# Kernel tuning notes

Hardware: AMD Instinct MI355X
Metric: run time of the kernel (lower is better)

## Reference

```python
import jax, jax.numpy as jnp
import numpy as np

NUM_HEADS = 16

def setup_inputs() -> dict:
    key = jax.random.key(0)
    k1, k2, k3 = jax.random.split(key, 3)
    B, S, H = 2, 2048, 1024
    x = jax.random.normal(k1, (B, S, H), dtype=jnp.float32)
    w_qkv = jax.random.normal(k2, (H, 3 * H), dtype=jnp.float32) * (1.0 / np.sqrt(H))
    w_out = jax.random.normal(k3, (H, H), dtype=jnp.float32) * (1.0 / np.sqrt(H))
    return {"x": x, "w_qkv": w_qkv, "w_out": w_out}

def reference(x, w_qkv, w_out):
    B, S, H = x.shape
    nh = NUM_HEADS
    dh = H // nh
    qkv = x @ w_qkv  # (B, S, 3H)
    q, k, v = jnp.split(qkv, 3, axis=-1)
    # (B, nh, S, dh)
    q = q.reshape(B, S, nh, dh).transpose(0, 2, 1, 3)
    k = k.reshape(B, S, nh, dh).transpose(0, 2, 1, 3)
    v = v.reshape(B, S, nh, dh).transpose(0, 2, 1, 3)
    att = jnp.einsum('bhsd,bhSd->bhsS', q, k) / np.sqrt(dh).astype(np.float32)
    causal = jnp.tril(jnp.ones((S, S), dtype=bool))
    att = jnp.where(causal[None, None], att, -jnp.inf)
    att = jax.nn.softmax(att, axis=-1)
    out = jnp.einsum('bhsS,bhSd->bhsd', att, v)
    out = out.transpose(0, 2, 1, 3).reshape(B, S, H)
    return out @ w_out
```

## Files before the change

### kernel.cpp

```cpp
#include <hip/hip_runtime.h>

#define DEVINL __device__ __forceinline__

typedef __attribute__((ext_vector_type(8)))  __bf16         bf16x8;
typedef __attribute__((ext_vector_type(4)))  float          f32x4;
typedef __attribute__((ext_vector_type(16))) float          f32x16;
typedef __attribute__((ext_vector_type(8)))  unsigned short ushort8;
typedef __attribute__((ext_vector_type(4)))  unsigned short ushort4v;
typedef __attribute__((ext_vector_type(4)))  unsigned int   uint4v;
typedef __attribute__((ext_vector_type(4)))  float          float4v;

DEVINL unsigned short f2bf(float f) {
  unsigned int u = __float_as_uint(f);
  u += 0x7fffu + ((u >> 16) & 1u);
  return (unsigned short)(u >> 16);
}

DEVINL float bf2f(unsigned short u) {
  return __uint_as_float(((unsigned int)u) << 16);
}

DEVINL bf16x8 ldbf8(const unsigned short* p) {
  return __builtin_bit_cast(bf16x8, *(const ushort8*)p);
}

DEVINL unsigned cvtpk_bf16(float lo, float hi) {
  unsigned r;
  asm("v_cvt_pk_bf16_f32 %0, %1, %2" : "=v"(r) : "v"(lo), "v"(hi));
  return r;
}

DEVINL void gload_lds16(const unsigned short* g, unsigned short* l) {
  __builtin_amdgcn_global_load_lds((const __attribute__((address_space(1))) void*)g,
                                   (__attribute__((address_space(3))) void*)l, 16, 0, 0);
}

__global__ __launch_bounds__(256) void prepass_kernel(
    const float* __restrict__ x, const float* __restrict__ w_qkv,
    const float* __restrict__ w_out, unsigned short* __restrict__ xb,
    unsigned short* __restrict__ wqkvT, unsigned short* __restrict__ woutT) {
  __shared__ float tile[32][33];
  const int B = blockIdx.x;
  if (B < 1024) {
    const int n4 = 1048576;
    for (int i = B * 256 + threadIdx.x; i < n4; i += 1024 * 256) {
      float4v v = *(const float4v*)(x + (size_t)4 * i);
      ushort4v o;
      o[0] = f2bf(v[0]); o[1] = f2bf(v[1]); o[2] = f2bf(v[2]); o[3] = f2bf(v[3]);
      *(ushort4v*)(xb + (size_t)4 * i) = o;
    }
    return;
  }
  const float* in; unsigned short* out; int C, bx, by;
  if (B < 4096) { const int idx = B - 1024; bx = idx % 96; by = idx / 96; in = w_qkv; out = wqkvT; C = 3072; }
  else          { const int idx = B - 4096; bx = idx & 31; by = idx >> 5; in = w_out; out = woutT; C = 1024; }
  const int R = 1024;
  const int tx = threadIdx.x & 31, ty = threadIdx.x >> 5;
  const int r0 = by << 5, c0 = bx << 5;
#pragma unroll
  for (int i = 0; i < 32; i += 8)
    tile[ty + i][tx] = in[(size_t)(r0 + ty + i) * C + (c0 + tx)];
  __syncthreads();
#pragma unroll
  for (int i = 0; i < 32; i += 8)
    out[(size_t)(c0 + ty + i) * R + (r0 + tx)] = f2bf(tile[tx][ty + i]);
}

template <bool OUT_BF16>
__global__ __launch_bounds__(256, 3) void gemm_bt_kernel(
    const unsigned short* __restrict__ A,
    const unsigned short* __restrict__ Bt,
    void* __restrict__ Cout,
    int M, int N, int K, int lda, int ldb, int ldc,
    unsigned short* __restrict__ VtOut) {
  __shared__ __align__(16) unsigned short smem[2][2][128 * 32];
  unsigned short (*As)[128 * 32] = smem[0];
  unsigned short (*Bs)[128 * 32] = smem[1];
  const int tid = threadIdx.x;
  const int lane = tid & 63, wave = tid >> 6;
  const int wr = wave >> 1, wc = wave & 1;
  const int g = lane >> 4, q = lane & 15;
  const int row0 = blockIdx.x << 7, col0 = blockIdx.y << 7;

  const int srow = tid >> 2;
  const int sg = ((tid & 3) ^ (srow & 3) ^ ((srow >> 2) & 3)) << 3;
  const unsigned short* Ap0 = A + (size_t)(row0 + srow) * lda + sg;
  const unsigned short* Ap1 = Ap0 + (size_t)64 * lda;
  const unsigned short* Bp0 = Bt + (size_t)(col0 + srow) * ldb + sg;
  const unsigned short* Bp1 = Bp0 + (size_t)64 * ldb;

  f32x4 acc[4][4] = {};

  gload_lds16(Ap0, &As[0][wave * 512]);
  gload_lds16(Ap1, &As[0][2048 + wave * 512]);
  gload_lds16(Bp0, &Bs[0][wave * 512]);
  gload_lds16(Bp1, &Bs[0][2048 + wave * 512]);

  const int gx = (g ^ (q & 3) ^ (q >> 2)) << 3;
  const int nk = K >> 5;
  int cur = 0;

  for (int t = 0; t < nk; ++t) {
    if (t + 1 < nk) {
      Ap0 += 32; Ap1 += 32; Bp0 += 32; Bp1 += 32;
      gload_lds16(Ap0, &As[cur ^ 1][wave * 512]);
      gload_lds16(Ap1, &As[cur ^ 1][2048 + wave * 512]);
      gload_lds16(Bp0, &Bs[cur ^ 1][wave * 512]);
      gload_lds16(Bp1, &Bs[cur ^ 1][2048 + wave * 512]);
      asm volatile("s_waitcnt vmcnt(4)" ::: "memory");
    } else {
      asm volatile("s_waitcnt vmcnt(0)" ::: "memory");
    }
    __builtin_amdgcn_s_barrier();

    bf16x8 af[4], bfr[4];
#pragma unroll
    for (int mb = 0; mb < 4; ++mb)
      af[mb] = ldbf8(&As[cur][(wr * 64 + mb * 16 + q) * 32] + gx);
#pragma unroll
    for (int nb = 0; nb < 4; ++nb)
      bfr[nb] = ldbf8(&Bs[cur][(wc * 64 + nb * 16 + q) * 32] + gx);
#pragma unroll
    for (int mb = 0; mb < 4; ++mb)
#pragma unroll
      for (int nb = 0; nb < 4; ++nb)
        acc[mb][nb] = __builtin_amdgcn_mfma_f32_16x16x32_bf16(af[mb], bfr[nb], acc[mb][nb], 0, 0, 0);

    __builtin_amdgcn_s_barrier();
    cur ^= 1;
  }

  const bool isV = OUT_BF16 && (VtOut != nullptr) && (col0 >= 2048);
  if (isV) {
    unsigned short* T = &smem[0][0][0];
    __syncthreads();
#pragma unroll
    for (int mb = 0; mb < 4; ++mb)
#pragma unroll
      for (int nb = 0; nb < 4; ++nb)
#pragma unroll
        for (int r = 0; r < 4; ++r) {
          const int sr = wr * 64 + mb * 16 + g * 4 + r;
          const int dc = wc * 64 + nb * 16 + q;
          T[dc * 128 + sr] = f2bf(acc[mb][nb][r]);
        }
    __syncthreads();
    const int d = tid >> 1, sh = (tid & 1) << 6;
    const int hI = ((col0 - 2048) >> 6) + (d >> 6), dI = d & 63;
    unsigned short* dst = VtOut + ((size_t)((row0 >> 11) * 16 + hI) * 64 + dI) * 2048 +
                          (row0 & 2047) + sh;
    const unsigned short* src = T + d * 128 + sh;
#pragma unroll
    for (int j = 0; j < 8; ++j)
      *(ushort8*)(dst + j * 8) = *(const ushort8*)(src + j * 8);
    return;
  }
#pragma unroll
  for (int mb = 0; mb < 4; ++mb)
#pragma unroll
    for (int nb = 0; nb < 4; ++nb)
#pragma unroll
      for (int r = 0; r < 4; ++r) {
        const int row = row0 + wr * 64 + mb * 16 + g * 4 + r;
        const int col = col0 + wc * 64 + nb * 16 + q;
        const float v = acc[mb][nb][r];
        if (OUT_BF16) ((unsigned short*)Cout)[(size_t)row * ldc + col] = f2bf(v);
        else          ((float*)Cout)[(size_t)row * ldc + col] = v;
      }
}

__global__ __launch_bounds__(256, 3) void gemm_bt64_kernel(
    const unsigned short* __restrict__ A,
    const unsigned short* __restrict__ Bt,
    float* __restrict__ Cout,
    int K, int lda, int ldb, int ldc) {
  __shared__ __align__(16) unsigned short As[2][64 * 32];
  __shared__ __align__(16) unsigned short Bs[2][128 * 32];
  const int tid = threadIdx.x;
  const int lane = tid & 63, wave = tid >> 6;
  const int wr = wave >> 1, wc = wave & 1;
  const int g = lane >> 4, q = lane & 15;
  const int row0 = blockIdx.x << 6, col0 = blockIdx.y << 7;

  const int srow = tid >> 2;
  const int sg = ((tid & 3) ^ (srow & 3) ^ ((srow >> 2) & 3)) << 3;
  const unsigned short* Ap = A + (size_t)(row0 + srow) * lda + sg;
  const unsigned short* Bp0 = Bt + (size_t)(col0 + srow) * ldb + sg;
  const unsigned short* Bp1 = Bp0 + (size_t)64 * ldb;

  f32x4 acc[2][4] = {};

  gload_lds16(Ap, &As[0][wave * 512]);
  gload_lds16(Bp0, &Bs[0][wave * 512]);
  gload_lds16(Bp1, &Bs[0][2048 + wave * 512]);

  const int gx = (g ^ (q & 3) ^ (q >> 2)) << 3;
  const int nk = K >> 5;
  int cur = 0;

  for (int t = 0; t < nk; ++t) {
    if (t + 1 < nk) {
      Ap += 32; Bp0 += 32; Bp1 += 32;
      gload_lds16(Ap, &As[cur ^ 1][wave * 512]);
      gload_lds16(Bp0, &Bs[cur ^ 1][wave * 512]);
      gload_lds16(Bp1, &Bs[cur ^ 1][2048 + wave * 512]);
      asm volatile("s_waitcnt vmcnt(3)" ::: "memory");
    } else {
      asm volatile("s_waitcnt vmcnt(0)" ::: "memory");
    }
    __builtin_amdgcn_s_barrier();

    bf16x8 af[2], bfr[4];
#pragma unroll
    for (int mb = 0; mb < 2; ++mb)
      af[mb] = ldbf8(&As[cur][(wr * 32 + mb * 16 + q) * 32] + gx);
#pragma unroll
    for (int nb = 0; nb < 4; ++nb)
      bfr[nb] = ldbf8(&Bs[cur][(wc * 64 + nb * 16 + q) * 32] + gx);
#pragma unroll
    for (int mb = 0; mb < 2; ++mb)
#pragma unroll
      for (int nb = 0; nb < 4; ++nb)
        acc[mb][nb] = __builtin_amdgcn_mfma_f32_16x16x32_bf16(af[mb], bfr[nb], acc[mb][nb], 0, 0, 0);

    __builtin_amdgcn_s_barrier();
    cur ^= 1;
  }

#pragma unroll
  for (int mb = 0; mb < 2; ++mb)
#pragma unroll
    for (int nb = 0; nb < 4; ++nb)
#pragma unroll
      for (int r = 0; r < 4; ++r) {
        const int row = row0 + wr * 32 + mb * 16 + g * 4 + r;
        const int col = col0 + wc * 64 + nb * 16 + q;
        Cout[(size_t)row * ldc + col] = acc[mb][nb][r];
      }
}

__global__ __launch_bounds__(256, 2) void attn_kernel(
    const unsigned short* __restrict__ qkv,
    const unsigned short* __restrict__ VtG,
    unsigned short* __restrict__ OlP,
    unsigned short* __restrict__ OhP,
    float* __restrict__ stats) {
  const int S = 2048, H = 1024, LD = 2048;
  const int tid = threadIdx.x;
  const int wave = tid >> 6, lane = tid & 63;
  const int c = lane & 31, hh = lane >> 5;

  const int L = blockIdx.x;
  const int group = L >> 8, r0_ = L & 255;
  const int pairid = r0_ & 7, bh = r0_ >> 3;
  const int qc = (group & 2) ? (15 - pairid) : pairid;
  const int half = group & 1;
  const int b = bh >> 4, h = bh & 15;
  const int q0w = qc * 128 + wave * 32;

  const unsigned short* Qb = qkv + (size_t)b * S * LD + h * 64;
  const unsigned short* Kb = Qb + 1024;
  const unsigned short* Vt = VtG + (size_t)(b * 16 + h) * 64 * S;

  __shared__ __align__(16) unsigned short Ks[2][64 * 64];
  __shared__ __align__(16) unsigned short Vs[2][64 * 64];

  const int srow = lane >> 3;
  const int srcg = ((lane & 7) ^ srow) << 3;
  const int wrow = wave * 8 + srow;

  const int nit = qc + 1;
  const int tb = half ? nit : 0;

  {
    const int cc = tb << 6;
    gload_lds16(Kb + (size_t)(cc + wrow) * LD + srcg,      Ks[0] + wave * 512);
    gload_lds16(Kb + (size_t)(cc + 32 + wrow) * LD + srcg, Ks[0] + 2048 + wave * 512);
    gload_lds16(Vt + (size_t)wrow * S + cc + srcg,         Vs[0] + wave * 512);
    gload_lds16(Vt + (size_t)(32 + wrow) * S + cc + srcg,  Vs[0] + 2048 + wave * 512);
  }

  bf16x8 qf[4];
#pragma unroll
  for (int kc = 0; kc < 4; ++kc)
    qf[kc] = ldbf8(Qb + (size_t)(q0w + c) * LD + kc * 16 + hh * 8);

  f32x16 acc[2] = {};
  float m_r = -1e30f, l_r = 0.f;
  const float CE = 0.125f * 1.44269504f;

  int cur = 0;
  const int swz = (c & 7) << 3;

  for (int t = 0; t < nit; ++t) {
    if (t + 1 < nit) {
      const int c1 = (tb + t + 1) << 6;
      unsigned short* KsN = Ks[cur ^ 1];
      unsigned short* VsN = Vs[cur ^ 1];
      gload_lds16(Kb + (size_t)(c1 + wrow) * LD + srcg,      KsN + wave * 512);
      gload_lds16(Kb + (size_t)(c1 + 32 + wrow) * LD + srcg, KsN + 2048 + wave * 512);
      gload_lds16(Vt + (size_t)wrow * S + c1 + srcg,         VsN + wave * 512);
      gload_lds16(Vt + (size_t)(32 + wrow) * S + c1 + srcg,  VsN + 2048 + wave * 512);
      asm volatile("s_waitcnt vmcnt(4)" ::: "memory");
    } else {
      asm volatile("s_waitcnt vmcnt(0)" ::: "memory");
    }
    __builtin_amdgcn_s_barrier();

    const int c0 = (tb + t) << 6;
    const unsigned short* KsC = Ks[cur];
    const unsigned short* VsC = Vs[cur];

    if (c0 <= q0w + 31) {
      int nv = ((q0w + 31 - c0) >> 5) + 1; if (nv > 2) nv = 2;

      bf16x8 kf[2][4];
#pragma unroll
      for (int n = 0; n < 2; ++n) if (n < nv)
#pragma unroll
        for (int kc = 0; kc < 4; ++kc)
          kf[n][kc] = ldbf8(KsC + (n * 32 + c) * 64 + ((kc * 16 + hh * 8) ^ swz));

      f32x16 st[2] = {};
      __builtin_amdgcn_s_setprio(1);
#pragma unroll
      for (int n = 0; n < 2; ++n) if (n < nv)
#pragma unroll
        for (int kc = 0; kc < 4; ++kc)
          st[n] = __builtin_amdgcn_mfma_f32_32x32x16_bf16(kf[n][kc], qf[kc], st[n], 0, 0, 0);
      __builtin_amdgcn_s_setprio(0);

      bf16x8 vf[2][4];
#pragma unroll
      for (int db = 0; db < 2; ++db)
#pragma unroll
        for (int kk = 0; kk < 4; ++kk) if (kk < 2 * nv)
          vf[db][kk] = ldbf8(VsC + (db * 32 + c) * 64 + ((kk * 16 + hh * 8) ^ swz));

      if (c0 + 63 > q0w) {
#pragma unroll
        for (int n = 0; n < 2; ++n) if (n < nv)
#pragma unroll
          for (int r = 0; r < 16; ++r) {
            const int kv = c0 + n * 32 + (r & 3) + 8 * (r >> 2) + 4 * hh;
            if (kv > q0w + c) st[n][r] = -1e30f;
          }
      }

      f32x4 pm = {-1e30f, -1e30f, -1e30f, -1e30f};
#pragma unroll
      for (int n = 0; n < 2; ++n) if (n < nv)
#pragma unroll
        for (int r = 0; r < 16; ++r) pm[r & 3] = fmaxf(pm[r & 3], st[n][r]);
      const float pmax = fmaxf(fmaxf(pm[0], pm[1]), fmaxf(pm[2], pm[3]));
      if (!__all(pmax <= m_r + 64.f)) {
        float px = fmaxf(pmax, __shfl_xor(pmax, 32));
        const float mn = fmaxf(m_r, px);
        const float sf = __builtin_amdgcn_exp2f((m_r - mn) * CE);
        m_r = mn; l_r *= sf;
#pragma unroll
        for (int db = 0; db < 2; ++db) acc[db] *= sf;
      }
      const float mC = m_r * CE;
      f32x4 la = {0.f, 0.f, 0.f, 0.f};
#pragma unroll
      for (int n = 0; n < 2; ++n) if (n < nv)
#pragma unroll
        for (int r = 0; r < 16; ++r) {
          const float p = __builtin_amdgcn_exp2f(fmaf(st[n][r], CE, -mC));
          st[n][r] = p;
          la[r & 3] += p;
        }
      l_r += (la[0] + la[1]) + (la[2] + la[3]);

      bf16x8 pa[4];
#pragma unroll
      for (int n = 0; n < 2; ++n) if (n < nv) {
        unsigned T0 = cvtpk_bf16(st[n][0],  st[n][1]);
        unsigned T1 = cvtpk_bf16(st[n][2],  st[n][3]);
        unsigned T2 = cvtpk_bf16(st[n][4],  st[n][5]);
        unsigned T3 = cvtpk_bf16(st[n][6],  st[n][7]);
        unsigned T4 = cvtpk_bf16(st[n][8],  st[n][9]);
        unsigned T5 = cvtpk_bf16(st[n][10], st[n][11]);
        unsigned T6 = cvtpk_bf16(st[n][12], st[n][13]);
        unsigned T7 = cvtpk_bf16(st[n][14], st[n][15]);
        asm("v_permlane32_swap_b32 %0, %1" : "+v"(T0), "+v"(T2));
        asm("v_permlane32_swap_b32 %0, %1" : "+v"(T1), "+v"(T3));
        asm("v_permlane32_swap_b32 %0, %1" : "+v"(T4), "+v"(T6));
        asm("v_permlane32_swap_b32 %0, %1" : "+v"(T5), "+v"(T7));
        uint4v w0; w0[0] = T0; w0[1] = T1; w0[2] = T2; w0[3] = T3;
        uint4v w1; w1[0] = T4; w1[1] = T5; w1[2] = T6; w1[3] = T7;
        pa[2 * n]     = __builtin_bit_cast(bf16x8, w0);
        pa[2 * n + 1] = __builtin_bit_cast(bf16x8, w1);
      }

      __builtin_amdgcn_s_setprio(1);
#pragma unroll
      for (int kk = 0; kk < 4; ++kk) if (kk < 2 * nv)
#pragma unroll
        for (int db = 0; db < 2; ++db)
          acc[db] = __builtin_amdgcn_mfma_f32_32x32x16_bf16(vf[db][kk], pa[kk], acc[db], 0, 0, 0);
      __builtin_amdgcn_s_setprio(0);
    }

    __builtin_amdgcn_s_barrier();
    cur ^= 1;
  }

  const float lt = l_r + __shfl_xor(l_r, 32);
  const float inv = lt > 0.f ? 1.f / lt : 0.f;
  unsigned short* Op = half ? OhP : OlP;
  const size_t rowbase = (size_t)(b * S + q0w + c) * H + h * 64;
#pragma unroll
  for (int db = 0; db < 2; ++db)
#pragma unroll
    for (int blk = 0; blk < 4; ++blk) {
      ushort4v o;
#pragma unroll
      for (int j = 0; j < 4; ++j) o[j] = f2bf(acc[db][blk * 4 + j] * inv);
      *(ushort4v*)(Op + rowbase + db * 32 + blk * 8 + hh * 4) = o;
    }
  if (hh == 0) {
    float* sp = stats + ((((size_t)(b * 16 + h)) << 11) + q0w + c) * 4 + (half ? 2 : 0);
    sp[0] = m_r; sp[1] = lt;
  }
}

__global__ __launch_bounds__(256) void attn_merge_kernel(
    const unsigned short* __restrict__ Ol,
    const unsigned short* __restrict__ Oh,
    const float* __restrict__ stats,
    unsigned short* __restrict__ Oout) {
  const float CE = 0.125f * 1.44269504f;
  const int i = blockIdx.x * 256 + threadIdx.x;
  const int r = i >> 7;
  const int g8 = i & 127;
  const int h = g8 >> 3;
  const int s = r & 2047, b = r >> 11;
  const float4v st = *(const float4v*)(stats + ((((size_t)(b * 16 + h)) << 11) + s) * 4);
  const float mn = fmaxf(st[0], st[2]);
  const float wl_ = st[1] * __builtin_amdgcn_exp2f((st[0] - mn) * CE);
  const float wh_ = st[3] * __builtin_amdgcn_exp2f((st[2] - mn) * CE);
  const float inv = 1.f / (wl_ + wh_);
  const float wl = wl_ * inv, wh = wh_ * inv;
  const size_t off = (size_t)i * 8;
  const ushort8 a = *(const ushort8*)(Ol + off);
  const ushort8 cc = *(const ushort8*)(Oh + off);
  ushort8 o;
#pragma unroll
  for (int j = 0; j < 8; ++j)
    o[j] = f2bf(wl * bf2f(a[j]) + wh * bf2f(cc[j]));
  *(ushort8*)(Oout + off) = o;
}

extern "C" void kernel_launch(void* const* d_in, const int* in_sizes, int n_in,
                              void* d_out, int out_size, void* d_ws, size_t ws_size,
                              hipStream_t stream) {
  const float* x     = (const float*)d_in[0];
  const float* w_qkv = (const float*)d_in[1];
  const float* w_out = (const float*)d_in[2];
  const int B = 2, S = 2048, H = 1024;
  const int M = B * S;

  unsigned short* xb    = (unsigned short*)d_ws;
  unsigned short* wqkvT = xb + (size_t)M * H;
  unsigned short* woutT = wqkvT + (size_t)3 * H * H;
  unsigned short* qkb   = woutT + (size_t)H * H;
  unsigned short* VtG   = qkb + (size_t)M * 2048;
  unsigned short* Ob    = VtG + (size_t)B * 16 * 64 * S;
  unsigned short* OhP   = xb;
  float*          stats = (float*)wqkvT;

  prepass_kernel<<<5120, 256, 0, stream>>>(x, w_qkv, w_out, xb, wqkvT, woutT);

  gemm_bt_kernel<true><<<dim3(M / 128, (3 * H) / 128), 256, 0, stream>>>(
      xb, wqkvT, qkb, M, 3 * H, H, H, H, 2048, VtG);

  attn_kernel<<<1024, 256, 0, stream>>>(qkb, VtG, Ob, OhP, stats);

  attn_merge_kernel<<<2048, 256, 0, stream>>>(Ob, OhP, stats, Ob);

  gemm_bt64_kernel<<<dim3(M / 64, H / 128), 256, 0, stream>>>(
      Ob, woutT, (float*)d_out, H, H, H, H);
}
```

Baseline: 114.5 us.

## Fuse split-KV merge into attention kernel via last-arriver atomic counter

Drops the separate merge kernel. Each attention block now bumps an atomic counter for its (batch-head, query chunk) tile, and whichever of the two halves finishes second combines both partial outputs using the saved max and sum stats. This saves a kernel launch and a full extra pass over the partial outputs. In exchange it adds thread fences, an atomic, and a memset of a counter buffer, which reuses the output buffer before the final GEMM overwrites it.

```diff
diff --git a/kernel.cpp b/kernel.cpp
--- a/kernel.cpp
+++ b/kernel.cpp
@@ -244,7 +244,8 @@
     const unsigned short* __restrict__ VtG,
     unsigned short* __restrict__ OlP,
     unsigned short* __restrict__ OhP,
-    float* __restrict__ stats) {
+    float* __restrict__ stats,
+    unsigned int* __restrict__ ctr) {
   const int S = 2048, H = 1024, LD = 2048;
   const int tid = threadIdx.x;
   const int wave = tid >> 6, lane = tid & 63;
@@ -424,33 +425,34 @@
     float* sp = stats + ((((size_t)(b * 16 + h)) << 11) + q0w + c) * 4 + (half ? 2 : 0);
     sp[0] = m_r; sp[1] = lt;
   }
-}
-
-__global__ __launch_bounds__(256) void attn_merge_kernel(
-    const unsigned short* __restrict__ Ol,
-    const unsigned short* __restrict__ Oh,
-    const float* __restrict__ stats,
-    unsigned short* __restrict__ Oout) {
-  const float CE = 0.125f * 1.44269504f;
-  const int i = blockIdx.x * 256 + threadIdx.x;
-  const int r = i >> 7;
-  const int g8 = i & 127;
-  const int h = g8 >> 3;
-  const int s = r & 2047, b = r >> 11;
-  const float4v st = *(const float4v*)(stats + ((((size_t)(b * 16 + h)) << 11) + s) * 4);
-  const float mn = fmaxf(st[0], st[2]);
-  const float wl_ = st[1] * __builtin_amdgcn_exp2f((st[0] - mn) * CE);
-  const float wh_ = st[3] * __builtin_amdgcn_exp2f((st[2] - mn) * CE);
-  const float inv = 1.f / (wl_ + wh_);
-  const float wl = wl_ * inv, wh = wh_ * inv;
-  const size_t off = (size_t)i * 8;
-  const ushort8 a = *(const ushort8*)(Ol + off);
-  const ushort8 cc = *(const ushort8*)(Oh + off);
-  ushort8 o;
-#pragma unroll
-  for (int j = 0; j < 8; ++j)
-    o[j] = f2bf(wl * bf2f(a[j]) + wh * bf2f(cc[j]));
-  *(ushort8*)(Oout + off) = o;
+
+  __threadfence();
+  __shared__ int sOld;
+  if (tid == 0) sOld = (int)atomicAdd(&ctr[(bh << 4) + qc], 1u);
+  __syncthreads();
+  if (sOld == 1) {
+    __threadfence();
+    const int row = tid >> 1;
+    const int col0m = (tid & 1) << 5;
+    const int sRow = qc * 128 + row;
+    const float* sp = stats + ((((size_t)bh) << 11) + sRow) * 4;
+    const float ml = sp[0], ll = sp[1], mh_ = sp[2], lh_ = sp[3];
+    const float mn = fmaxf(ml, mh_);
+    const float a_ = ll * __builtin_amdgcn_exp2f((ml - mn) * CE);
+    const float b_ = lh_ * __builtin_amdgcn_exp2f((mh_ - mn) * CE);
+    const float iv = 1.f / (a_ + b_);
+    const float wl = a_ * iv, wh_ = b_ * iv;
+    const size_t base = (size_t)(b * S + sRow) * H + h * 64 + col0m;
+#pragma unroll
+    for (int j = 0; j < 4; ++j) {
+      const ushort8 lo = *(const ushort8*)(OlP + base + j * 8);
+      const ushort8 hi = *(const ushort8*)(OhP + base + j * 8);
+      ushort8 o;
+#pragma unroll
+      for (int e = 0; e < 8; ++e) o[e] = f2bf(wl * bf2f(lo[e]) + wh_ * bf2f(hi[e]));
+      *(ushort8*)(OlP + base + j * 8) = o;
+    }
+  }
 }
 
 extern "C" void kernel_launch(void* const* d_in, const int* in_sizes, int n_in,
@@ -470,15 +472,16 @@
   unsigned short* Ob    = VtG + (size_t)B * 16 * 64 * S;
   unsigned short* OhP   = xb;
   float*          stats = (float*)wqkvT;
+  unsigned int*   ctr   = (unsigned int*)d_out;
+
+  hipMemsetAsync(ctr, 0, 512 * sizeof(unsigned int), stream);
 
   prepass_kernel<<<5120, 256, 0, stream>>>(x, w_qkv, w_out, xb, wqkvT, woutT);
 
   gemm_bt_kernel<true><<<dim3(M / 128, (3 * H) / 128), 256, 0, stream>>>(
       xb, wqkvT, qkb, M, 3 * H, H, H, H, 2048, VtG);
 
-  attn_kernel<<<1024, 256, 0, stream>>>(qkb, VtG, Ob, OhP, stats);
-
-  attn_merge_kernel<<<2048, 256, 0, stream>>>(Ob, OhP, stats, Ob);
+  attn_kernel<<<1024, 256, 0, stream>>>(qkb, VtG, Ob, OhP, stats, ctr);
 
   gemm_bt64_kernel<<<dim3(M / 64, H / 128), 256, 0, stream>>>(
       Ob, woutT, (float*)d_out, H, H, H, H);
```

After: 327.5 us. 186% more time.
